# Kernel optimization log

Hardware: AMD Instinct MI355X
Metric: run time of the kernel (lower is better)

Reference implementation:

```python
import jax, jax.numpy as jnp
import numpy as np

N_NODES = 50000
N_GRAPHS = 512
HID = 128
IN = 128
SLOPE = 0.2  # LeakyReLU negative slope (PyG default)


def _gatv2(x, src, dst, Wl, bl, Wr, br, att, bias, n):
    # PyG GATv2Conv, 1 head: xl used for source/messages, xr for targets
    xl = x @ Wl + bl          # [N, H]
    xr = x @ Wr + br          # [N, H]
    # per-edge score: att . LeakyReLU(xl[j] + xr[i])
    e = jax.nn.leaky_relu(xl[src] + xr[dst], SLOPE) @ att  # [E]
    # softmax grouped by destination node (self loops guarantee nonempty groups)
    m = jax.ops.segment_max(e, dst, num_segments=n)
    p = jnp.exp(e - m[dst])
    s = jax.ops.segment_sum(p, dst, num_segments=n)
    alpha = p / s[dst]                                      # [E]
    out = jax.ops.segment_sum(alpha[:, None] * xl[src], dst, num_segments=n)
    return out + bias


def setup_inputs() -> dict:
    key = jax.random.key(0)
    ks = jax.random.split(key, 24)
    x = jax.random.normal(ks[0], (N_NODES, IN), jnp.float32)
    edge_index = jax.random.randint(ks[1], (2, 1600000), 0, N_NODES, jnp.int64)
    batch = jnp.sort(jax.random.randint(ks[2], (N_NODES,), 0, N_GRAPHS, jnp.int64))

    def lin(k, fi, fo):
        k1, k2 = jax.random.split(k)
        sc = 1.0 / np.sqrt(fi)
        return (jax.random.uniform(k1, (fi, fo), jnp.float32, -sc, sc),
                jax.random.uniform(k2, (fo,), jnp.float32, -sc, sc))

    d = {"x": x, "edge_index": edge_index, "batch": batch}
    dims = [(IN, HID), (HID, HID), (HID, HID)]
    for i, (fi, fo) in enumerate(dims, 1):
        Wl, bl = lin(ks[3 * i], fi, fo)
        Wr, br = lin(ks[3 * i + 1], fi, fo)
        d[f"Wl{i}"], d[f"bl{i}"] = Wl, bl
        d[f"Wr{i}"], d[f"br{i}"] = Wr, br
        d[f"att{i}"] = jax.random.normal(ks[3 * i + 2], (fo,), jnp.float32) / np.sqrt(fo)
        d[f"bias{i}"] = jnp.zeros((fo,), jnp.float32)
    d["W4"], d["b4"] = lin(ks[15], HID, 128)
    d["W5"], d["b5"] = lin(ks[16], 128, 64)
    d["W6"], d["b6"] = lin(ks[17], 64, 2)
    return d


def reference(x, edge_index, batch,
              Wl1, bl1, Wr1, br1, att1, bias1,
              Wl2, bl2, Wr2, br2, att2, bias2,
              Wl3, bl3, Wr3, br3, att3, bias3,
              W4, b4, W5, b5, W6, b6):
    n = x.shape[0]
    loop = jnp.arange(n, dtype=edge_index.dtype)
    src = jnp.concatenate([edge_index[0], loop])  # add_self_loops=True
    dst = jnp.concatenate([edge_index[1], loop])

    h = jax.nn.relu(_gatv2(x, src, dst, Wl1, bl1, Wr1, br1, att1, bias1, n))
    h = jax.nn.relu(_gatv2(h, src, dst, Wl2, bl2, Wr2, br2, att2, bias2, n))
    h = _gatv2(h, src, dst, Wl3, bl3, Wr3, br3, att3, bias3, n)

    # global_mean_pool over graph ids
    sums = jax.ops.segment_sum(h, batch, num_segments=N_GRAPHS)
    cnts = jax.ops.segment_sum(jnp.ones((n,), h.dtype), batch, num_segments=N_GRAPHS)
    g = sums / jnp.maximum(cnts, 1.0)[:, None]

    # dropout is identity in eval mode; MLP head
    g = jax.nn.sigmoid(g @ W4 + b4)
    g = jax.nn.sigmoid(g @ W5 + b5)
    return g @ W6 + b6
```

## Files before the change

### kernel.cpp

```cpp
#include <hip/hip_runtime.h>
#include <hip/hip_bf16.h>
#include <math.h>

#define BK_SHIFT 7
#define BK_NODES 128

typedef _Float16 h2 __attribute__((ext_vector_type(2)));
typedef _Float16 f16x8 __attribute__((ext_vector_type(8)));
typedef float f32x4 __attribute__((ext_vector_type(4)));

__device__ __forceinline__ h2 u2h(unsigned u){ return __builtin_bit_cast(h2, u); }

__device__ __forceinline__ int dev_lower_bound(const int* __restrict__ a, int n, int v){
  int lo = 0, hi = n;
  while (lo < hi){ int mid = (lo + hi) >> 1; if (a[mid] < v) lo = mid + 1; else hi = mid; }
  return lo;
}

__global__ __launch_bounds__(256) void p1_bucket_count(const int* __restrict__ edst,
    int* __restrict__ bktTotal, int nE, int K){
  __shared__ int cnt[512];
  for (int k = threadIdx.x; k < K; k += 256) cnt[k] = 0;
  __syncthreads();
  int i = (blockIdx.x * 256 + threadIdx.x) * 8;
  if (i + 7 < nE){
    int4 a = *(const int4*)(edst + i);
    int4 b = *(const int4*)(edst + i + 4);
    atomicAdd(&cnt[a.x >> BK_SHIFT], 1); atomicAdd(&cnt[a.y >> BK_SHIFT], 1);
    atomicAdd(&cnt[a.z >> BK_SHIFT], 1); atomicAdd(&cnt[a.w >> BK_SHIFT], 1);
    atomicAdd(&cnt[b.x >> BK_SHIFT], 1); atomicAdd(&cnt[b.y >> BK_SHIFT], 1);
    atomicAdd(&cnt[b.z >> BK_SHIFT], 1); atomicAdd(&cnt[b.w >> BK_SHIFT], 1);
  } else {
    for (int j = i; j < nE; ++j) atomicAdd(&cnt[edst[j] >> BK_SHIFT], 1);
  }
  __syncthreads();
  for (int k = threadIdx.x; k < K; k += 256)
    if (cnt[k]) atomicAdd(&bktTotal[k], cnt[k]);
}

__global__ __launch_bounds__(512) void p2_scan(const int* __restrict__ bktTotal,
    int* __restrict__ bktBase, int* __restrict__ bktCur,
    int* __restrict__ row_off, int K, int n, int nE){
  __shared__ int sh[512];
  int t = threadIdx.x;
  int v = (t < K) ? bktTotal[t] : 0;
  sh[t] = v;
  __syncthreads();
  for (int off = 1; off < 512; off <<= 1){
    int u = (t >= off) ? sh[t - off] : 0;
    __syncthreads();
    sh[t] += u;
    __syncthreads();
  }
  if (t < K){
    int excl = sh[t] - v;
    bktBase[t] = excl;
    bktCur[t]  = excl;
  }
  if (t == 0){
    bktBase[K] = nE;
    row_off[n] = nE + n;
  }
}

__global__ __launch_bounds__(256) void p3_partition(const int* __restrict__ esrc,
    const int* __restrict__ edst, int* __restrict__ bktCur,
    int2* __restrict__ ebuf, int nE, int K){
  __shared__ int cnt[512];
  __shared__ int base[512];
  for (int k = threadIdx.x; k < K; k += 256) cnt[k] = 0;
  __syncthreads();
  const int i0 = (blockIdx.x * 256 + threadIdx.x) * 8;
  const int i1 = min(i0 + 8, nE);
  int bkt[8];
  int sv[8], dv[8];
  int cnt_local = i1 - i0;
  for (int j = 0; j < cnt_local; ++j){
    sv[j] = esrc[i0 + j];
    dv[j] = edst[i0 + j];
    bkt[j] = dv[j] >> BK_SHIFT;
    atomicAdd(&cnt[bkt[j]], 1);
  }
  __syncthreads();
  for (int k = threadIdx.x; k < K; k += 256){
    int c = cnt[k];
    base[k] = c ? atomicAdd(&bktCur[k], c) : 0;
  }
  __syncthreads();
  for (int k = threadIdx.x; k < K; k += 256) cnt[k] = 0;
  __syncthreads();
  for (int j = 0; j < cnt_local; ++j){
    int r = atomicAdd(&cnt[bkt[j]], 1);
    ebuf[base[bkt[j]] + r] = make_int2(sv[j], dv[j]);
  }
}

__global__ __launch_bounds__(256) void p4_build(const int2* __restrict__ ebuf,
    const int* __restrict__ bktBase, int* __restrict__ row_off,
    int* __restrict__ csr_src, int n){
  const int b = blockIdx.x;
  const int node0 = b << BK_SHIFT;
  const int nNodes = min(BK_NODES, n - node0);
  const int tid = threadIdx.x;
  __shared__ int ldeg[BK_NODES];
  __shared__ int lcur[BK_NODES];
  __shared__ int sc[BK_NODES];
  const int e0 = bktBase[b];
  const int e1 = bktBase[b + 1];
  if (tid < BK_NODES) ldeg[tid] = 0;
  __syncthreads();
  for (int i = e0 + tid; i < e1; i += 256)
    atomicAdd(&ldeg[ebuf[i].y - node0], 1);
  __syncthreads();
  if (tid < BK_NODES) sc[tid] = (tid < nNodes) ? (ldeg[tid] + 1) : 0;
  __syncthreads();
  for (int off = 1; off < BK_NODES; off <<= 1){
    int u = 0;
    if (tid < BK_NODES && tid >= off) u = sc[tid - off];
    __syncthreads();
    if (tid < BK_NODES) sc[tid] += u;
    __syncthreads();
  }
  if (tid < nNodes){
    const int csr0 = e0 + node0;
    int ro = csr0 + sc[tid] - (ldeg[tid] + 1);
    row_off[node0 + tid] = ro;
    lcur[tid] = ro;
  }
  __syncthreads();
  for (int i = e0 + tid; i < e1; i += 256){
    int2 e = ebuf[i];
    int p = atomicAdd(&lcur[e.y - node0], 1);
    csr_src[p] = e.x;
  }
  __syncthreads();
  if (tid < nNodes)
    csr_src[lcur[tid]] = node0 + tid;
}

__global__ __launch_bounds__(256) void prep_w_kernel(
    const float* __restrict__ W0, const float* __restrict__ W1,
    const float* __restrict__ W2, const float* __restrict__ W3,
    const float* __restrict__ W4m, const float* __restrict__ W5m,
    unsigned short* __restrict__ Wt16)
{
  const float* Ws[6] = {W0, W1, W2, W3, W4m, W5m};
  const int mat = blockIdx.x >> 3;
  const int chunk = blockIdx.x & 7;
  const float* W = Ws[mat];
  unsigned short* o = Wt16 + mat * 16384;
  #pragma unroll
  for (int e = 0; e < 8; ++e){
    int i = chunk * 2048 + e * 256 + threadIdx.x;
    int k = i >> 7, col = i & 127;
    _Float16 h = (_Float16)W[i];
    o[col * 128 + k] = __builtin_bit_cast(unsigned short, h);
  }
}

__global__ __launch_bounds__(256) void gemm_mfma_kernel(
    const float* __restrict__ X,
    const unsigned short* __restrict__ WtL,
    const float* __restrict__ bl, const float* __restrict__ br,
    unsigned short* __restrict__ xl16, unsigned short* __restrict__ xr16, int n)
{
  const int mat = blockIdx.y;
  const unsigned short* Wt = WtL + mat * 16384;
  const float* bias = mat ? br : bl;
  unsigned short* out = mat ? xr16 : xl16;
  const int w   = threadIdx.x >> 6;
  const int l   = threadIdx.x & 63;
  const int l15 = l & 15;
  const int kq  = l >> 4;
  const int rowbase = blockIdx.x * 128 + w * 32;

  f16x8 a[2][4];
  #pragma unroll
  for (int rt = 0; rt < 2; ++rt){
    const int r = rowbase + rt * 16 + l15;
    const bool ok = r < n;
    const float* src = X + (size_t)min(r, n - 1) * 128 + kq * 8;
    #pragma unroll
    for (int ks = 0; ks < 4; ++ks){
      float4 f0 = ok ? *(const float4*)(src + ks * 32)     : make_float4(0.f,0.f,0.f,0.f);
      float4 f1 = ok ? *(const float4*)(src + ks * 32 + 4) : make_float4(0.f,0.f,0.f,0.f);
      f16x8 v;
      v[0] = (_Float16)f0.x; v[1] = (_Float16)f0.y;
      v[2] = (_Float16)f0.z; v[3] = (_Float16)f0.w;
      v[4] = (_Float16)f1.x; v[5] = (_Float16)f1.y;
      v[6] = (_Float16)f1.z; v[7] = (_Float16)f1.w;
      a[rt][ks] = v;
    }
  }

  f32x4 acc[2][8];
  #pragma unroll
  for (int rt = 0; rt < 2; ++rt)
    #pragma unroll
    for (int ct = 0; ct < 8; ++ct)
      acc[rt][ct] = (f32x4){0.f, 0.f, 0.f, 0.f};

  #pragma unroll
  for (int ks = 0; ks < 4; ++ks){
    #pragma unroll
    for (int ct = 0; ct < 8; ++ct){
      f16x8 b = *(const f16x8*)(Wt + (size_t)(ct * 16 + l15) * 128 + ks * 32 + kq * 8);
      acc[0][ct] = __builtin_amdgcn_mfma_f32_16x16x32_f16(a[0][ks], b, acc[0][ct], 0, 0, 0);
      acc[1][ct] = __builtin_amdgcn_mfma_f32_16x16x32_f16(a[1][ks], b, acc[1][ct], 0, 0, 0);
    }
  }

  #pragma unroll
  for (int ct = 0; ct < 8; ++ct){
    const float bv = bias[ct * 16 + l15];
    #pragma unroll
    for (int rt = 0; rt < 2; ++rt){
      #pragma unroll
      for (int rg = 0; rg < 4; ++rg){
        const int r = rowbase + rt * 16 + kq * 4 + rg;
        if (r < n){
          _Float16 h = (_Float16)(acc[rt][ct][rg] + bv);
          out[(size_t)r * 128 + ct * 16 + l15] = __builtin_bit_cast(unsigned short, h);
        }
      }
    }
  }
}

__global__ __launch_bounds__(256) void edge_attn_kernel(
    const unsigned short* __restrict__ xl16, const unsigned short* __restrict__ xr16,
    const int* __restrict__ row_off, const int* __restrict__ csr_src,
    const float* __restrict__ att, const float* __restrict__ bias,
    float* __restrict__ out, int n, int do_relu)
{
  const int node = (blockIdx.x * blockDim.x + threadIdx.x) >> 4;
  const int nodec = min(node, n - 1);
  const int lane16 = threadIdx.x & 15;
  const int f8 = lane16 * 8;

  const uint4 xru = *(const uint4*)(xr16 + (size_t)nodec * 128 + f8);
  const h2 xr0 = u2h(xru.x), xr1 = u2h(xru.y), xr2 = u2h(xru.z), xr3 = u2h(xru.w);
  const float4 aA = *(const float4*)(att + f8);
  const float4 aB = *(const float4*)(att + f8 + 4);
  const h2 at0 = {(_Float16)aA.x, (_Float16)aA.y};
  const h2 at1 = {(_Float16)aA.z, (_Float16)aA.w};
  const h2 at2 = {(_Float16)aB.x, (_Float16)aB.y};
  const h2 at3 = {(_Float16)aB.z, (_Float16)aB.w};
  const h2 k02 = {(_Float16)0.2f, (_Float16)0.2f};

  const int base = row_off[nodec];
  const int deg  = row_off[nodec + 1] - base;
  int dmax = max(deg, __shfl_xor(deg, 16));
  dmax = max(dmax, __shfl_xor(dmax, 32));

  auto part = [&](uint4 xp) -> float {
    h2 u0 = u2h(xp.x) + xr0;
    h2 u1 = u2h(xp.y) + xr1;
    h2 u2 = u2h(xp.z) + xr2;
    h2 u3 = u2h(xp.w) + xr3;
    u0 = __builtin_elementwise_max(u0, u0 * k02);
    u1 = __builtin_elementwise_max(u1, u1 * k02);
    u2 = __builtin_elementwise_max(u2, u2 * k02);
    u3 = __builtin_elementwise_max(u3, u3 * k02);
    float ps = __builtin_amdgcn_fdot2(u0, at0, 0.f, false);
    ps = __builtin_amdgcn_fdot2(u1, at1, ps, false);
    ps = __builtin_amdgcn_fdot2(u2, at2, ps, false);
    ps = __builtin_amdgcn_fdot2(u3, at3, ps, false);
    return ps;
  };

  uint4 xp = *(const uint4*)(xl16 + (size_t)csr_src[base] * 128 + f8);
  float p = part(xp);
  p += __shfl_xor(p, 1); p += __shfl_xor(p, 2);
  p += __shfl_xor(p, 4); p += __shfl_xor(p, 8);
  float m = p, Mrun = p, s = 1.f;
  float a0 = (float)u2h(xp.x).x, a1 = (float)u2h(xp.x).y;
  float a2 = (float)u2h(xp.y).x, a3 = (float)u2h(xp.y).y;
  float a4 = (float)u2h(xp.z).x, a5 = (float)u2h(xp.z).y;
  float a6 = (float)u2h(xp.w).x, a7 = (float)u2h(xp.w).y;

  for (int it = 1; it < dmax; it += 4){
    const int c0 = min(it,     deg - 1);
    const int c1 = min(it + 1, deg - 1);
    const int c2 = min(it + 2, deg - 1);
    const int c3 = min(it + 3, deg - 1);
    const int s0 = csr_src[base + c0];
    const int s1 = csr_src[base + c1];
    const int s2 = csr_src[base + c2];
    const int s3 = csr_src[base + c3];
    const uint4 xA = *(const uint4*)(xl16 + (size_t)s0 * 128 + f8);
    const uint4 xB = *(const uint4*)(xl16 + (size_t)s1 * 128 + f8);
    const uint4 xC = *(const uint4*)(xl16 + (size_t)s2 * 128 + f8);
    const uint4 xD = *(const uint4*)(xl16 + (size_t)s3 * 128 + f8);
    float pA = part(xA), pB = part(xB), pC = part(xC), pD = part(xD);
    #pragma unroll
    for (int off = 1; off < 16; off <<= 1){
      pA += __shfl_xor(pA, off);
      pB += __shfl_xor(pB, off);
      pC += __shfl_xor(pC, off);
      pD += __shfl_xor(pD, off);
    }
    const bool vA = it < deg, vB = it + 1 < deg, vC = it + 2 < deg, vD = it + 3 < deg;
    float fA = vA ? pA : -3.0e38f;
    float fB = vB ? pB : -3.0e38f;
    float fC = vC ? pC : -3.0e38f;
    float fD = vD ? pD : -3.0e38f;
    Mrun = fmaxf(Mrun, fmaxf(fmaxf(fA, fB), fmaxf(fC, fD)));
    if (__any(Mrun > m + 8.f)){
      float sc = __expf(m - Mrun);
      s *= sc;
      a0 *= sc; a1 *= sc; a2 *= sc; a3 *= sc;
      a4 *= sc; a5 *= sc; a6 *= sc; a7 *= sc;
      m = Mrun;
    }
    float qA = vA ? __expf(pA - m) : 0.f;
    float qB = vB ? __expf(pB - m) : 0.f;
    float qC = vC ? __expf(pC - m) : 0.f;
    float qD = vD ? __expf(pD - m) : 0.f;
    s += (qA + qB) + (qC + qD);
    h2 w;
    w = u2h(xA.x); a0 = fmaf(qA, (float)w.x, a0); a1 = fmaf(qA, (float)w.y, a1);
    w = u2h(xA.y); a2 = fmaf(qA, (float)w.x, a2); a3 = fmaf(qA, (float)w.y, a3);
    w = u2h(xA.z); a4 = fmaf(qA, (float)w.x, a4); a5 = fmaf(qA, (float)w.y, a5);
    w = u2h(xA.w); a6 = fmaf(qA, (float)w.x, a6); a7 = fmaf(qA, (float)w.y, a7);
    w = u2h(xB.x); a0 = fmaf(qB, (float)w.x, a0); a1 = fmaf(qB, (float)w.y, a1);
    w = u2h(xB.y); a2 = fmaf(qB, (float)w.x, a2); a3 = fmaf(qB, (float)w.y, a3);
    w = u2h(xB.z); a4 = fmaf(qB, (float)w.x, a4); a5 = fmaf(qB, (float)w.y, a5);
    w = u2h(xB.w); a6 = fmaf(qB, (float)w.x, a6); a7 = fmaf(qB, (float)w.y, a7);
    w = u2h(xC.x); a0 = fmaf(qC, (float)w.x, a0); a1 = fmaf(qC, (float)w.y, a1);
    w = u2h(xC.y); a2 = fmaf(qC, (float)w.x, a2); a3 = fmaf(qC, (float)w.y, a3);
    w = u2h(xC.z); a4 = fmaf(qC, (float)w.x, a4); a5 = fmaf(qC, (float)w.y, a5);
    w = u2h(xC.w); a6 = fmaf(qC, (float)w.x, a6); a7 = fmaf(qC, (float)w.y, a7);
    w = u2h(xD.x); a0 = fmaf(qD, (float)w.x, a0); a1 = fmaf(qD, (float)w.y, a1);
    w = u2h(xD.y); a2 = fmaf(qD, (float)w.x, a2); a3 = fmaf(qD, (float)w.y, a3);
    w = u2h(xD.z); a4 = fmaf(qD, (float)w.x, a4); a5 = fmaf(qD, (float)w.y, a5);
    w = u2h(xD.w); a6 = fmaf(qD, (float)w.x, a6); a7 = fmaf(qD, (float)w.y, a7);
  }

  if (node < n){
    const float inv = 1.0f / s;
    const float4 bA = *(const float4*)(bias + f8);
    const float4 bB = *(const float4*)(bias + f8 + 4);
    float o0 = fmaf(a0, inv, bA.x), o1 = fmaf(a1, inv, bA.y);
    float o2 = fmaf(a2, inv, bA.z), o3 = fmaf(a3, inv, bA.w);
    float o4 = fmaf(a4, inv, bB.x), o5 = fmaf(a5, inv, bB.y);
    float o6 = fmaf(a6, inv, bB.z), o7 = fmaf(a7, inv, bB.w);
    if (do_relu){
      o0 = fmaxf(o0, 0.f); o1 = fmaxf(o1, 0.f); o2 = fmaxf(o2, 0.f); o3 = fmaxf(o3, 0.f);
      o4 = fmaxf(o4, 0.f); o5 = fmaxf(o5, 0.f); o6 = fmaxf(o6, 0.f); o7 = fmaxf(o7, 0.f);
    }
    *(float4*)(out + (size_t)node * 128 + f8)     = make_float4(o0, o1, o2, o3);
    *(float4*)(out + (size_t)node * 128 + f8 + 4) = make_float4(o4, o5, o6, o7);
  }
}

__global__ __launch_bounds__(128) void pool_mlp_kernel(
    const float* __restrict__ h, const int* __restrict__ batch, int n,
    const float* __restrict__ W4, const float* __restrict__ b4,
    const float* __restrict__ W5, const float* __restrict__ b5,
    const float* __restrict__ W6, const float* __restrict__ b6,
    float* __restrict__ out)
{
  int g = blockIdx.x;
  int t = threadIdx.x;
  __shared__ float gf[128];
  __shared__ float h1[128];
  __shared__ float h2s[64];
  int lo = dev_lower_bound(batch, n, g);
  int hi = dev_lower_bound(batch, n, g + 1);
  float ssum = 0.f;
  for (int i = lo; i < hi; ++i) ssum += h[(size_t)i * 128 + t];
  float cnt = (float)(hi - lo);
  gf[t] = ssum / fmaxf(cnt, 1.0f);
  __syncthreads();
  float a = b4[t];
  for (int k = 0; k < 128; ++k) a = fmaf(gf[k], W4[k * 128 + t], a);
  h1[t] = 1.0f / (1.0f + __expf(-a));
  __syncthreads();
  if (t < 64){
    float a5 = b5[t];
    for (int k = 0; k < 128; ++k) a5 = fmaf(h1[k], W5[k * 64 + t], a5);
    h2s[t] = 1.0f / (1.0f + __expf(-a5));
  }
  __syncthreads();
  if (t < 2){
    float a6 = b6[t];
    for (int k = 0; k < 64; ++k) a6 = fmaf(h2s[k], W6[k * 2 + t], a6);
    out[g * 2 + t] = a6;
  }
}

extern "C" void kernel_launch(void* const* d_in, const int* in_sizes, int n_in,
                              void* d_out, int out_size, void* d_ws, size_t ws_size,
                              hipStream_t stream)
{
  const float* x          = (const float*)d_in[0];
  const int*   edge_index = (const int*)d_in[1];
  const int*   batch      = (const int*)d_in[2];
  const int n  = in_sizes[0] / 128;
  const int nE = in_sizes[1] / 2;
  const int* esrc = edge_index;
  const int* edst = edge_index + nE;
  const int n_graphs = out_size / 2;
  const int K = (n + BK_NODES - 1) >> BK_SHIFT;

  const float *Wl[3], *bl[3], *Wr[3], *br[3], *att[3], *bias[3];
  for (int l = 0; l < 3; ++l){
    Wl[l]   = (const float*)d_in[3 + 6 * l + 0];
    bl[l]   = (const float*)d_in[3 + 6 * l + 1];
    Wr[l]   = (const float*)d_in[3 + 6 * l + 2];
    br[l]   = (const float*)d_in[3 + 6 * l + 3];
    att[l]  = (const float*)d_in[3 + 6 * l + 4];
    bias[l] = (const float*)d_in[3 + 6 * l + 5];
  }
  const float* W4 = (const float*)d_in[21]; const float* b4 = (const float*)d_in[22];
  const float* W5 = (const float*)d_in[23]; const float* b5 = (const float*)d_in[24];
  const float* W6 = (const float*)d_in[25]; const float* b6 = (const float*)d_in[26];

  char* ws = (char*)d_ws;
  size_t off = 0;
  auto alloc = [&](size_t bytes) -> void* {
    void* p = ws + off;
    off = (off + bytes + 255) & ~(size_t)255;
    return p;
  };
  int*   row_off  = (int*)  alloc((size_t)(n + 1) * sizeof(int));
  int*   bktTotal = (int*)  alloc(512 * sizeof(int));
  int*   bktBase  = (int*)  alloc(513 * sizeof(int));
  int*   bktCur   = (int*)  alloc(512 * sizeof(int));
  int*   csr_src  = (int*)  alloc((size_t)(nE + n) * sizeof(int));
  int2*  ebuf     = (int2*) alloc((size_t)nE * sizeof(int2));
  unsigned short* xlb16 = (unsigned short*)alloc((size_t)n * 128 * sizeof(unsigned short));
  unsigned short* xrb16 = (unsigned short*)alloc((size_t)n * 128 * sizeof(unsigned short));
  unsigned short* Wt16  = (unsigned short*)alloc(6 * 16384 * sizeof(unsigned short));
  float* hC       = (float*)alloc((size_t)n * 128 * sizeof(float));
  (void)ws_size; (void)n_in;

  prep_w_kernel<<<48, 256, 0, stream>>>(Wl[0], Wr[0], Wl[1], Wr[1], Wl[2], Wr[2], Wt16);

  hipMemsetAsync(bktTotal, 0, 512 * sizeof(int), stream);
  const int eblocks = (nE + 2048 - 1) / 2048;
  p1_bucket_count<<<eblocks, 256, 0, stream>>>(edst, bktTotal, nE, K);
  p2_scan<<<1, 512, 0, stream>>>(bktTotal, bktBase, bktCur, row_off, K, n, nE);
  p3_partition<<<eblocks, 256, 0, stream>>>(esrc, edst, bktCur, ebuf, nE, K);
  p4_build<<<K, 256, 0, stream>>>(ebuf, bktBase, row_off, csr_src, n);

  const int gemm_tiles = (n + 127) / 128;
  const int attn_blocks = (int)(((size_t)n * 16 + 255) / 256);

  gemm_mfma_kernel<<<dim3(gemm_tiles, 2), 256, 0, stream>>>(x, Wt16 + 0 * 32768,
                                                            bl[0], br[0], xlb16, xrb16, n);
  edge_attn_kernel<<<attn_blocks, 256, 0, stream>>>(xlb16, xrb16, row_off, csr_src,
                                                    att[0], bias[0], hC, n, 1);
  gemm_mfma_kernel<<<dim3(gemm_tiles, 2), 256, 0, stream>>>(hC, Wt16 + 1 * 32768,
                                                            bl[1], br[1], xlb16, xrb16, n);
  edge_attn_kernel<<<attn_blocks, 256, 0, stream>>>(xlb16, xrb16, row_off, csr_src,
                                                    att[1], bias[1], hC, n, 1);
  gemm_mfma_kernel<<<dim3(gemm_tiles, 2), 256, 0, stream>>>(hC, Wt16 + 2 * 32768,
                                                            bl[2], br[2], xlb16, xrb16, n);
  edge_attn_kernel<<<attn_blocks, 256, 0, stream>>>(xlb16, xrb16, row_off, csr_src,
                                                    att[2], bias[2], hC, n, 0);

  pool_mlp_kernel<<<n_graphs, 128, 0, stream>>>(hC, batch, n, W4, b4, W5, b5, W6, b6,
                                                (float*)d_out);
}
```

Baseline: 435.3 us.

## Sort nodes by degree for attention load balance and store hidden states as fp16

```diff
diff --git a/kernel.cpp b/kernel.cpp
--- a/kernel.cpp
+++ b/kernel.cpp
@@ -136,6 +136,55 @@
   __syncthreads();
   if (tid < nNodes)
     csr_src[lcur[tid]] = node0 + tid;
+}
+
+__global__ __launch_bounds__(256) void deg_hist(const int* __restrict__ row_off,
+    int* __restrict__ dbins, int n){
+  __shared__ int cnt[256];
+  cnt[threadIdx.x] = 0;
+  __syncthreads();
+  int i = blockIdx.x * 256 + threadIdx.x;
+  if (i < n){
+    int deg = row_off[i + 1] - row_off[i];
+    atomicAdd(&cnt[min(deg, 255)], 1);
+  }
+  __syncthreads();
+  if (cnt[threadIdx.x]) atomicAdd(&dbins[threadIdx.x], cnt[threadIdx.x]);
+}
+
+__global__ __launch_bounds__(256) void deg_scan(const int* __restrict__ dbins,
+    int* __restrict__ dcur){
+  __shared__ int sh[256];
+  int t = threadIdx.x;
+  int v = dbins[t];
+  sh[t] = v;
+  __syncthreads();
+  for (int off = 1; off < 256; off <<= 1){
+    int u = (t >= off) ? sh[t - off] : 0;
+    __syncthreads();
+    sh[t] += u;
+    __syncthreads();
+  }
+  dcur[t] = sh[t] - v;
+}
+
+__global__ __launch_bounds__(256) void deg_scatter(const int* __restrict__ row_off,
+    int* __restrict__ dcur, int* __restrict__ order, int n){
+  __shared__ int cnt[256];
+  __shared__ int base[256];
+  cnt[threadIdx.x] = 0;
+  __syncthreads();
+  int i = blockIdx.x * 256 + threadIdx.x;
+  int bin = 0, r = 0;
+  if (i < n){
+    int deg = row_off[i + 1] - row_off[i];
+    bin = min(deg, 255);
+    r = atomicAdd(&cnt[bin], 1);
+  }
+  __syncthreads();
+  base[threadIdx.x] = cnt[threadIdx.x] ? atomicAdd(&dcur[threadIdx.x], cnt[threadIdx.x]) : 0;
+  __syncthreads();
+  if (i < n) order[base[bin] + r] = i;
 }
 
 __global__ __launch_bounds__(256) void prep_w_kernel(
@@ -158,8 +207,9 @@
   }
 }
 
+template<bool F16IN>
 __global__ __launch_bounds__(256) void gemm_mfma_kernel(
-    const float* __restrict__ X,
+    const void* __restrict__ Xv,
     const unsigned short* __restrict__ WtL,
     const float* __restrict__ bl, const float* __restrict__ br,
     unsigned short* __restrict__ xl16, unsigned short* __restrict__ xr16, int n)
@@ -179,17 +229,24 @@
   for (int rt = 0; rt < 2; ++rt){
     const int r = rowbase + rt * 16 + l15;
     const bool ok = r < n;
-    const float* src = X + (size_t)min(r, n - 1) * 128 + kq * 8;
+    const int rc = min(r, n - 1);
     #pragma unroll
     for (int ks = 0; ks < 4; ++ks){
-      float4 f0 = ok ? *(const float4*)(src + ks * 32)     : make_float4(0.f,0.f,0.f,0.f);
-      float4 f1 = ok ? *(const float4*)(src + ks * 32 + 4) : make_float4(0.f,0.f,0.f,0.f);
-      f16x8 v;
-      v[0] = (_Float16)f0.x; v[1] = (_Float16)f0.y;
-      v[2] = (_Float16)f0.z; v[3] = (_Float16)f0.w;
-      v[4] = (_Float16)f1.x; v[5] = (_Float16)f1.y;
-      v[6] = (_Float16)f1.z; v[7] = (_Float16)f1.w;
-      a[rt][ks] = v;
+      if (F16IN){
+        const unsigned short* src = (const unsigned short*)Xv + (size_t)rc * 128 + kq * 8 + ks * 32;
+        f16x8 v = ok ? *(const f16x8*)src : (f16x8){0,0,0,0,0,0,0,0};
+        a[rt][ks] = v;
+      } else {
+        const float* src = (const float*)Xv + (size_t)rc * 128 + kq * 8 + ks * 32;
+        float4 f0 = ok ? *(const float4*)(src)     : make_float4(0.f,0.f,0.f,0.f);
+        float4 f1 = ok ? *(const float4*)(src + 4) : make_float4(0.f,0.f,0.f,0.f);
+        f16x8 v;
+        v[0] = (_Float16)f0.x; v[1] = (_Float16)f0.y;
+        v[2] = (_Float16)f0.z; v[3] = (_Float16)f0.w;
+        v[4] = (_Float16)f1.x; v[5] = (_Float16)f1.y;
+        v[6] = (_Float16)f1.z; v[7] = (_Float16)f1.w;
+        a[rt][ks] = v;
+      }
     }
   }
 
@@ -230,15 +287,16 @@
 __global__ __launch_bounds__(256) void edge_attn_kernel(
     const unsigned short* __restrict__ xl16, const unsigned short* __restrict__ xr16,
     const int* __restrict__ row_off, const int* __restrict__ csr_src,
+    const int* __restrict__ order,
     const float* __restrict__ att, const float* __restrict__ bias,
-    float* __restrict__ out, int n, int do_relu)
+    unsigned short* __restrict__ out16, int n, int do_relu)
 {
-  const int node = (blockIdx.x * blockDim.x + threadIdx.x) >> 4;
-  const int nodec = min(node, n - 1);
+  const int gid = (blockIdx.x * blockDim.x + threadIdx.x) >> 4;
+  const int node = order[min(gid, n - 1)];
   const int lane16 = threadIdx.x & 15;
   const int f8 = lane16 * 8;
 
-  const uint4 xru = *(const uint4*)(xr16 + (size_t)nodec * 128 + f8);
+  const uint4 xru = *(const uint4*)(xr16 + (size_t)node * 128 + f8);
   const h2 xr0 = u2h(xru.x), xr1 = u2h(xru.y), xr2 = u2h(xru.z), xr3 = u2h(xru.w);
   const float4 aA = *(const float4*)(att + f8);
   const float4 aB = *(const float4*)(att + f8 + 4);
@@ -248,8 +306,8 @@
   const h2 at3 = {(_Float16)aB.z, (_Float16)aB.w};
   const h2 k02 = {(_Float16)0.2f, (_Float16)0.2f};
 
-  const int base = row_off[nodec];
-  const int deg  = row_off[nodec + 1] - base;
+  const int base = row_off[node];
+  const int deg  = row_off[node + 1] - base;
   int dmax = max(deg, __shfl_xor(deg, 16));
   dmax = max(dmax, __shfl_xor(dmax, 32));
 
@@ -337,7 +395,7 @@
     w = u2h(xD.w); a6 = fmaf(qD, (float)w.x, a6); a7 = fmaf(qD, (float)w.y, a7);
   }
 
-  if (node < n){
+  if (gid < n){
     const float inv = 1.0f / s;
     const float4 bA = *(const float4*)(bias + f8);
     const float4 bB = *(const float4*)(bias + f8 + 4);
@@ -349,13 +407,22 @@
       o0 = fmaxf(o0, 0.f); o1 = fmaxf(o1, 0.f); o2 = fmaxf(o2, 0.f); o3 = fmaxf(o3, 0.f);
       o4 = fmaxf(o4, 0.f); o5 = fmaxf(o5, 0.f); o6 = fmaxf(o6, 0.f); o7 = fmaxf(o7, 0.f);
     }
-    *(float4*)(out + (size_t)node * 128 + f8)     = make_float4(o0, o1, o2, o3);
-    *(float4*)(out + (size_t)node * 128 + f8 + 4) = make_float4(o4, o5, o6, o7);
+    ushort4 wlo, whi;
+    wlo.x = __builtin_bit_cast(unsigned short, (_Float16)o0);
+    wlo.y = __builtin_bit_cast(unsigned short, (_Float16)o1);
+    wlo.z = __builtin_bit_cast(unsigned short, (_Float16)o2);
+    wlo.w = __builtin_bit_cast(unsigned short, (_Float16)o3);
+    whi.x = __builtin_bit_cast(unsigned short, (_Float16)o4);
+    whi.y = __builtin_bit_cast(unsigned short, (_Float16)o5);
+    whi.z = __builtin_bit_cast(unsigned short, (_Float16)o6);
+    whi.w = __builtin_bit_cast(unsigned short, (_Float16)o7);
+    *(ushort4*)(out16 + (size_t)node * 128 + f8)     = wlo;
+    *(ushort4*)(out16 + (size_t)node * 128 + f8 + 4) = whi;
   }
 }
 
 __global__ __launch_bounds__(128) void pool_mlp_kernel(
-    const float* __restrict__ h, const int* __restrict__ batch, int n,
+    const unsigned short* __restrict__ h, const int* __restrict__ batch, int n,
     const float* __restrict__ W4, const float* __restrict__ b4,
     const float* __restrict__ W5, const float* __restrict__ b5,
     const float* __restrict__ W6, const float* __restrict__ b6,
@@ -369,7 +436,10 @@
   int lo = dev_lower_bound(batch, n, g);
   int hi = dev_lower_bound(batch, n, g + 1);
   float ssum = 0.f;
-  for (int i = lo; i < hi; ++i) ssum += h[(size_t)i * 128 + t];
+  for (int i = lo; i < hi; ++i){
+    _Float16 hv = __builtin_bit_cast(_Float16, h[(size_t)i * 128 + t]);
+    ssum += (float)hv;
+  }
   float cnt = (float)(hi - lo);
   gf[t] = ssum / fmaxf(cnt, 1.0f);
   __syncthreads();
@@ -428,39 +498,48 @@
   int*   bktTotal = (int*)  alloc(512 * sizeof(int));
   int*   bktBase  = (int*)  alloc(513 * sizeof(int));
   int*   bktCur   = (int*)  alloc(512 * sizeof(int));
+  int*   dbins    = (int*)  alloc(256 * sizeof(int));
+  int*   dcur     = (int*)  alloc(256 * sizeof(int));
+  int*   order    = (int*)  alloc((size_t)n * sizeof(int));
   int*   csr_src  = (int*)  alloc((size_t)(nE + n) * sizeof(int));
   int2*  ebuf     = (int2*) alloc((size_t)nE * sizeof(int2));
   unsigned short* xlb16 = (unsigned short*)alloc((size_t)n * 128 * sizeof(unsigned short));
   unsigned short* xrb16 = (unsigned short*)alloc((size_t)n * 128 * sizeof(unsigned short));
   unsigned short* Wt16  = (unsigned short*)alloc(6 * 16384 * sizeof(unsigned short));
-  float* hC       = (float*)alloc((size_t)n * 128 * sizeof(float));
+  unsigned short* hC16  = (unsigned short*)alloc((size_t)n * 128 * sizeof(unsigned short));
   (void)ws_size; (void)n_in;
 
   prep_w_kernel<<<48, 256, 0, stream>>>(Wl[0], Wr[0], Wl[1], Wr[1], Wl[2], Wr[2], Wt16);
 
   hipMemsetAsync(bktTotal, 0, 512 * sizeof(int), stream);
+  hipMemsetAsync(dbins, 0, 256 * sizeof(int), stream);
   const int eblocks = (nE + 2048 - 1) / 2048;
   p1_bucket_count<<<eblocks, 256, 0, stream>>>(edst, bktTotal, nE, K);
   p2_scan<<<1, 512, 0, stream>>>(bktTotal, bktBase, bktCur, row_off, K, n, nE);
   p3_partition<<<eblocks, 256, 0, stream>>>(esrc, edst, bktCur, ebuf, nE, K);
   p4_build<<<K, 256, 0, stream>>>(ebuf, bktBase, row_off, csr_src, n);
 
+  const int nblocks = (n + 255) / 256;
+  deg_hist<<<nblocks, 256, 0, stream>>>(row_off, dbins, n);
+  deg_scan<<<1, 256, 0, stream>>>(dbins, dcur);
+  deg_scatter<<<nblocks, 256, 0, stream>>>(row_off, dcur, order, n);
+
   const int gemm_tiles = (n + 127) / 128;
   const int attn_blocks = (int)(((size_t)n * 16 + 255) / 256);
 
-  gemm_mfma_kernel<<<dim3(gemm_tiles, 2), 256, 0, stream>>>(x, Wt16 + 0 * 32768,
+  gemm_mfma_kernel<false><<<dim3(gemm_tiles, 2), 256, 0, stream>>>(x, Wt16 + 0 * 32768,
                                                             bl[0], br[0], xlb16, xrb16, n);
-  edge_attn_kernel<<<attn_blocks, 256, 0, stream>>>(xlb16, xrb16, row_off, csr_src,
-                                                    att[0], bias[0], hC, n, 1);
-  gemm_mfma_kernel<<<dim3(gemm_tiles, 2), 256, 0, stream>>>(hC, Wt16 + 1 * 32768,
+  edge_attn_kernel<<<attn_blocks, 256, 0, stream>>>(xlb16, xrb16, row_off, csr_src, order,
+                                                    att[0], bias[0], hC16, n, 1);
+  gemm_mfma_kernel<true><<<dim3(gemm_tiles, 2), 256, 0, stream>>>(hC16, Wt16 + 1 * 32768,
                                                             bl[1], br[1], xlb16, xrb16, n);
-  edge_attn_kernel<<<attn_blocks, 256, 0, stream>>>(xlb16, xrb16, row_off, csr_src,
-                                                    att[1], bias[1], hC, n, 1);
-  gemm_mfma_kernel<<<dim3(gemm_tiles, 2), 256, 0, stream>>>(hC, Wt16 + 2 * 32768,
+  edge_attn_kernel<<<attn_blocks, 256, 0, stream>>>(xlb16, xrb16, row_off, csr_src, order,
+                                                    att[1], bias[1], hC16, n, 1);
+  gemm_mfma_kernel<true><<<dim3(gemm_tiles, 2), 256, 0, stream>>>(hC16, Wt16 + 2 * 32768,
                                                             bl[2], br[2], xlb16, xrb16, n);
-  edge_attn_kernel<<<attn_blocks, 256, 0, stream>>>(xlb16, xrb16, row_off, csr_src,
-                                                    att[2], bias[2], hC, n, 0);
-
-  pool_mlp_kernel<<<n_graphs, 128, 0, stream>>>(hC, batch, n, W4, b4, W5, b5, W6, b6,
+  edge_attn_kernel<<<attn_blocks, 256, 0, stream>>>(xlb16, xrb16, row_off, csr_src, order,
+                                                    att[2], bias[2], hC16, n, 0);
+
+  pool_mlp_kernel<<<n_graphs, 128, 0, stream>>>(hC16, batch, n, W4, b4, W5, b5, W6, b6,
                                                 (float*)d_out);
 }
```

After: 431.8 us. No clear change (-0.8%).
